# Kernel tuning notes

Hardware: AMD Instinct MI355X
Metric: run time of the kernel (lower is better)

Reference implementation:

```python
import jax, jax.numpy as jnp
import numpy as np

DIM = 768
N_HEADS = 12
HEAD_DIM = DIM // N_HEADS
SCALE = HEAD_DIM ** -0.5


def setup_inputs() -> dict:
    key = jax.random.key(0)
    ks = jax.random.split(key, 5)
    x = jax.random.normal(ks[0], (8, 1024, DIM), dtype=jnp.float32)
    w_qkv = jax.random.normal(ks[1], (DIM, 3 * DIM), dtype=jnp.float32) * (DIM ** -0.5)
    b_qkv = jnp.zeros((3 * DIM,), dtype=jnp.float32)
    w_proj = jax.random.normal(ks[2], (DIM, DIM), dtype=jnp.float32) * (DIM ** -0.5)
    b_proj = jnp.zeros((DIM,), dtype=jnp.float32)
    return {"x": x, "w_qkv": w_qkv, "b_qkv": b_qkv, "w_proj": w_proj, "b_proj": b_proj}


def reference(x, w_qkv, b_qkv, w_proj, b_proj):
    B, N, _ = x.shape
    qkv = x @ w_qkv + b_qkv                       # [B, N, 3*DIM]
    qkv = qkv.reshape(B, N, 3, N_HEADS, HEAD_DIM)
    q = qkv[:, :, 0].transpose(0, 2, 1, 3)        # [B, H, N, D]
    k = qkv[:, :, 1].transpose(0, 2, 1, 3)
    v = qkv[:, :, 2].transpose(0, 2, 1, 3)
    attn = jnp.einsum('bhnd,bhmd->bhnm', q, k) * SCALE
    attn = jax.nn.softmax(attn, axis=-1)
    out = jnp.einsum('bhnm,bhmd->bhnd', attn, v)  # [B, H, N, D]
    out = out.transpose(0, 2, 1, 3).reshape(B, N, DIM)
    return out @ w_proj + b_proj
```

## Files before the change

### kernel.cpp

```cpp
#include <hip/hip_runtime.h>
#include <hip/hip_bf16.h>

#define NHEADS 12
#define HDIM   64
#define SEQ    1024
#define NBATCH 8
#define MODELD 768
#define QKVD   2304
#define BHEADS (NBATCH * NHEADS)

typedef __attribute__((ext_vector_type(8))) short          bf16x8;
typedef __attribute__((ext_vector_type(8))) unsigned short u16x8;
typedef __attribute__((ext_vector_type(4))) unsigned short u16x4;
typedef __attribute__((ext_vector_type(4))) float          f32x4;

static __device__ __forceinline__ unsigned short f2bf(float f) {
  unsigned int u = __float_as_uint(f);
  u += 0x7fffu + ((u >> 16) & 1u);
  return (unsigned short)(u >> 16);
}

static __device__ __forceinline__ unsigned int pk2(float x, float y) {
  __hip_bfloat162 h = __float22bfloat162_rn(make_float2(x, y));
  return *(unsigned int*)&h;
}

static __device__ __forceinline__ void gld_lds16(const void* g, void* l) {
  __builtin_amdgcn_global_load_lds((const __attribute__((address_space(1))) void*)g,
                                   (__attribute__((address_space(3))) void*)l, 16, 0, 0);
}

#define QSC 0.18033688f

static __device__ __forceinline__ void transpose_body(
    const float* __restrict__ in, unsigned short* __restrict__ out,
    int R, int C, int bx, int by, int tid) {
  __shared__ float t[32][33];
  const int c0 = bx * 32, r0 = by * 32;
  const int lr = tid >> 3;
  const int lc = (tid & 7) * 4;
  const float* p = in + (size_t)(r0 + lr) * C + c0 + lc;
  float4 v = *(const float4*)p;
  t[lr][lc]     = v.x;
  t[lr][lc + 1] = v.y;
  t[lr][lc + 2] = v.z;
  t[lr][lc + 3] = v.w;
  __syncthreads();
  unsigned short* q = out + (size_t)(c0 + lr) * R + r0 + lc;
  q[0] = f2bf(t[lc][lr]);
  q[1] = f2bf(t[lc + 1][lr]);
  q[2] = f2bf(t[lc + 2][lr]);
  q[3] = f2bf(t[lc + 3][lr]);
}

__global__ __launch_bounds__(256) void prep(
    const float* __restrict__ x, unsigned short* __restrict__ Xb,
    const float* __restrict__ w_qkv, unsigned short* __restrict__ wqkvT,
    const float* __restrict__ w_proj, unsigned short* __restrict__ wprojT) {
  const int id = blockIdx.x;
  const int tid = threadIdx.x;
  if (id < 3072) {
    const int i = (id * 256 + tid) * 8;
    const float4 a0 = *(const float4*)(x + i);
    const float4 a1 = *(const float4*)(x + i + 4);
    union { unsigned int u[4]; u16x8 v; } w;
    w.u[0] = pk2(a0.x, a0.y); w.u[1] = pk2(a0.z, a0.w);
    w.u[2] = pk2(a1.x, a1.y); w.u[3] = pk2(a1.z, a1.w);
    *(u16x8*)(Xb + i) = w.v;
  } else if (id < 4800) {
    const int u = id - 3072;
    transpose_body(w_qkv, wqkvT, MODELD, QKVD, u % 72, u / 72, tid);
  } else {
    const int u = id - 4800;
    transpose_body(w_proj, wprojT, MODELD, MODELD, u % 24, u / 24, tid);
  }
}

#define GEMM_CORE(AP, BP)                                                      \
  const int tid  = threadIdx.x;                                                \
  const int lane = tid & 63;                                                   \
  const int wave = tid >> 6;                                                   \
  const int wm = wave >> 1, wn = wave & 1;                                     \
  const int fr = lane & 15;                                                    \
  const int fq = lane >> 4;                                                    \
  const int swz = (fr & 7) << 4;                                               \
  const int srow8 = lane >> 3;                                                 \
  const int scb8 = (((lane & 7) ^ srow8) << 4);                                \
  f32x4 acc[4][4] = {};                                                        \
  auto stA = [&](int dbuf, int kb, int R) {                                    \
    gld_lds16(AP + (size_t)(R + srow8) * 1536 + kb + scb8,                     \
              (char*)smem + dbuf * 16384 + R * 128);                           \
  };                                                                           \
  auto stB = [&](int dbuf, int kb, int R) {                                    \
    gld_lds16(BP + (size_t)(R + srow8) * 1536 + kb + scb8,                     \
              (char*)smem + 32768 + dbuf * 16384 + R * 128);                   \
  };                                                                           \
  _Pragma("unroll")                                                            \
  for (int pt = 0; pt < 2; ++pt) {                                             \
    const int kb = pt * 128;                                                   \
    stA(pt, kb, wave * 8);      stA(pt, kb, 32 + wave * 8);                    \
    stA(pt, kb, 64 + wave * 8); stA(pt, kb, 96 + wave * 8);                    \
    stB(pt, kb, wave * 8);      stB(pt, kb, 64 + wave * 8);                    \
    stB(pt, kb, 32 + wave * 8); stB(pt, kb, 96 + wave * 8);                    \
  }                                                                            \
  asm volatile("s_waitcnt vmcnt(8)" ::: "memory");                             \
  __builtin_amdgcn_s_barrier();                                                \
  for (int kt = 0; kt < 12; ++kt) {                                            \
    const int db = kt & 1;                                                     \
    const char* Ad = (const char*)smem + db * 16384;                           \
    const char* Bd = (const char*)smem + 32768 + db * 16384;                   \
    bf16x8 a[4][2], b[4][2];                                                   \
    _Pragma("unroll")                                                          \
    for (int i = 0; i < 4; ++i)                                                \
      _Pragma("unroll")                                                        \
      for (int c = 0; c < 2; ++c)                                              \
        a[i][c] = *(const bf16x8*)(Ad + (wm * 64 + i * 16 + fr) * 128 +        \
                                   ((c * 64 + fq * 16) ^ swz));                \
    _Pragma("unroll")                                                          \
    for (int j = 0; j < 2; ++j)                                                \
      _Pragma("unroll")                                                        \
      for (int c = 0; c < 2; ++c)                                              \
        b[j][c] = *(const bf16x8*)(Bd + (wn * 64 + j * 16 + fr) * 128 +        \
                                   ((c * 64 + fq * 16) ^ swz));                \
    if (kt >= 1 && kt <= 10) {                                                 \
      stB(db ^ 1, (kt + 1) * 128, 32 + wave * 8);                              \
      stB(db ^ 1, (kt + 1) * 128, 96 + wave * 8);                              \
    }                                                                          \
    if (kt < 11) asm volatile("s_waitcnt vmcnt(8)" ::: "memory");              \
    else         asm volatile("s_waitcnt vmcnt(0)" ::: "memory");              \
    __builtin_amdgcn_s_barrier();                                              \
    __builtin_amdgcn_s_setprio(1);                                             \
    _Pragma("unroll")                                                          \
    for (int i = 0; i < 4; ++i)                                                \
      _Pragma("unroll")                                                        \
      for (int j = 0; j < 2; ++j)                                              \
        _Pragma("unroll")                                                      \
        for (int c = 0; c < 2; ++c)                                            \
          acc[i][j] = __builtin_amdgcn_mfma_f32_16x16x32_bf16(                 \
              a[i][c], b[j][c], acc[i][j], 0, 0, 0);                           \
    __builtin_amdgcn_s_setprio(0);                                             \
    __builtin_amdgcn_s_barrier();                                              \
    _Pragma("unroll")                                                          \
    for (int j = 0; j < 2; ++j)                                                \
      _Pragma("unroll")                                                        \
      for (int c = 0; c < 2; ++c)                                              \
        b[2 + j][c] = *(const bf16x8*)(Bd + (wn * 64 + (2 + j) * 16 + fr) *    \
                                       128 + ((c * 64 + fq * 16) ^ swz));      \
    if (kt <= 9) {                                                             \
      const int kb2 = (kt + 2) * 128;                                          \
      stA(db, kb2, wave * 8);      stA(db, kb2, 32 + wave * 8);                \
      stA(db, kb2, 64 + wave * 8); stA(db, kb2, 96 + wave * 8);                \
      stB(db, kb2, wave * 8);      stB(db, kb2, 64 + wave * 8);                \
    }                                                                          \
    if (kt <= 9)       asm volatile("s_waitcnt vmcnt(6)" ::: "memory");        \
    else if (kt == 10) asm volatile("s_waitcnt vmcnt(2)" ::: "memory");        \
    else               asm volatile("s_waitcnt vmcnt(0)" ::: "memory");        \
    __builtin_amdgcn_s_barrier();                                              \
    __builtin_amdgcn_s_setprio(1);                                             \
    _Pragma("unroll")                                                          \
    for (int i = 0; i < 4; ++i)                                                \
      _Pragma("unroll")                                                        \
      for (int j = 0; j < 2; ++j)                                              \
        _Pragma("unroll")                                                      \
        for (int c = 0; c < 2; ++c)                                            \
          acc[i][2 + j] = __builtin_amdgcn_mfma_f32_16x16x32_bf16(             \
              a[i][c], b[2 + j][c], acc[i][2 + j], 0, 0, 0);                   \
    __builtin_amdgcn_s_setprio(0);                                             \
    __builtin_amdgcn_s_barrier();                                              \
  }

__global__ __launch_bounds__(256, 2) void gemm_qkv(
    const unsigned short* __restrict__ Xb, const unsigned short* __restrict__ WT,
    const float* __restrict__ bias,
    unsigned short* __restrict__ Qo, unsigned short* __restrict__ Ko,
    unsigned short* __restrict__ VTo) {
  __shared__ __align__(16) unsigned short smem[32768];
  int flat = blockIdx.x;
  flat = (flat & 7) * 144 + (flat >> 3);
  const int m0 = (flat / 18) * 128;
  const int n0 = (flat % 18) * 128;
  const char* Ap = (const char*)(Xb + (size_t)m0 * MODELD);
  const char* Bp = (const char*)(WT + (size_t)n0 * MODELD);

  GEMM_CORE(Ap, Bp)

  __builtin_amdgcn_s_barrier();
  const int wr = wm * 64, wc = wn * 64;
  const int s = n0 / MODELD;
  if (s < 2) {
    const float qs = (s == 0) ? QSC : 1.0f;
#pragma unroll
    for (int i = 0; i < 4; ++i) {
#pragma unroll
      for (int j = 0; j < 4; ++j) {
        const int col = n0 + wc + j * 16 + fr;
        const int rem = col - s * MODELD;
        const int h = rem >> 6, d = rem & 63;
        const float bv = bias[col];
#pragma unroll
        for (int r = 0; r < 4; ++r) {
          const int row = m0 + wr + i * 16 + fq * 4 + r;
          const int bb = row >> 10, n = row & 1023;
          const int bh = bb * NHEADS + h;
          const unsigned short val = f2bf((acc[i][j][r] + bv) * qs);
          if (s == 0) Qo[((size_t)bh * SEQ + n) * HDIM + d] = val;
          else        Ko[((size_t)bh * SEQ + n) * HDIM + d] = val;
        }
      }
    }
  } else {
    unsigned short* T = smem + wave * 4608;
#pragma unroll
    for (int i = 0; i < 4; ++i) {
#pragma unroll
      for (int j = 0; j < 4; ++j) {
        const int col = n0 + wc + j * 16 + fr;
        const float bv = bias[col];
        const int dl = j * 16 + fr;
        union { unsigned int u[2]; u16x4 v; } pk;
        pk.u[0] = pk2(acc[i][j][0] + bv, acc[i][j][1] + bv);
        pk.u[1] = pk2(acc[i][j][2] + bv, acc[i][j][3] + bv);
        *(u16x4*)&T[dl * 72 + i * 16 + fq * 4] = pk.v;
      }
    }
    asm volatile("s_waitcnt lgkmcnt(0)" ::: "memory");
    const int h  = (n0 + wc - 2 * MODELD) >> 6;
    const int rowb = m0 + wr;
    const int bb = rowb >> 10, nq = rowb & 1023;
    const int bh = bb * NHEADS + h;
    unsigned short* Vb = VTo + ((size_t)bh * HDIM) * SEQ + nq;
#pragma unroll
    for (int u = 0; u < 8; ++u) {
      const int d  = u * 8 + (lane >> 3);
      const int qc = (lane & 7) * 8;
      u16x8 v = *(const u16x8*)&T[d * 72 + qc];
      *(u16x8*)(Vb + (size_t)d * SEQ + qc) = v;
    }
  }
}

__global__ __launch_bounds__(256, 2) void gemm_proj(
    const unsigned short* __restrict__ A, const unsigned short* __restrict__ WT,
    const float* __restrict__ bias, float* __restrict__ Out) {
  __shared__ __align__(16) unsigned short smem[32768];
  int flat = blockIdx.x;
  flat = (flat & 7) * 48 + (flat >> 3);
  const int m0 = (flat / 6) * 128;
  const int n0 = (flat % 6) * 128;
  const char* Ap = (const char*)(A  + (size_t)m0 * MODELD);
  const char* Bp = (const char*)(WT + (size_t)n0 * MODELD);

  GEMM_CORE(Ap, Bp)

  const int wr = wm * 64, wc = wn * 64;
#pragma unroll
  for (int i = 0; i < 4; ++i) {
#pragma unroll
    for (int j = 0; j < 4; ++j) {
      const int col = n0 + wc + j * 16 + fr;
      const float bv = bias[col];
#pragma unroll
      for (int r = 0; r < 4; ++r) {
        const int row = m0 + wr + i * 16 + fq * 4 + r;
        Out[(size_t)row * MODELD + col] = acc[i][j][r] + bv;
      }
    }
  }
}

__global__ __launch_bounds__(256, 3) void attn_fused(
    const unsigned short* __restrict__ Q, const unsigned short* __restrict__ K,
    const unsigned short* __restrict__ VT, unsigned short* __restrict__ AO) {
  __shared__ __align__(16) unsigned short smem[24576];

  const int tid  = threadIdx.x;
  const int lane = tid & 63;
  const int wave = tid >> 6;

  const int flat = blockIdx.y * 8 + blockIdx.x;
  const int xcd = flat & 7, j = flat >> 3;
  const int bh = xcd * 12 + (j >> 3);
  const int qb = j & 7;
  const int b = bh / NHEADS, h = bh % NHEADS;
  const int q0 = qb * 128 + wave * 32;

  const unsigned short* Qp = Q  + (size_t)bh * SEQ * HDIM;
  const unsigned short* Kp = K  + (size_t)bh * SEQ * HDIM;
  const unsigned short* Vp = VT + (size_t)bh * HDIM * SEQ;

  const int fr = lane & 15;
  const int fq = lane >> 4;
  const int swz = (fr & 7) << 4;

  bf16x8 qf[2][2];
#pragma unroll
  for (int g = 0; g < 2; ++g)
#pragma unroll
    for (int c = 0; c < 2; ++c)
      qf[g][c] = *(const bf16x8*)(Qp + (size_t)(q0 + g * 16 + fr) * HDIM + c * 32 + fq * 8);

  const int srow_lo = (lane >> 3);
  const int scx = (((lane & 7) ^ srow_lo) << 4);

  f32x4 acc[2][4] = {};
  f32x4 accl[2] = {};
  bf16x8 ones;
#pragma unroll
  for (int i = 0; i < 8; ++i) ones[i] = (short)0x3F80;

  auto stage = [&](int buf, int kv0) {
    const char* Kb = (const char*)Kp + (size_t)kv0 * 128;
    const char* Vb = (const char*)Vp + (size_t)kv0 * 2;
#pragma unroll
    for (int u = 0; u < 2; ++u) {
      const int i = wave * 2 + u;
      const int r0 = i * 8 + srow_lo;
      gld_lds16(Kb + (size_t)r0 * 128  + scx, (char*)smem + buf * 8192 + i * 1024);
      gld_lds16(Vb + (size_t)r0 * 2048 + scx, (char*)smem + 24576 + buf * 8192 + i * 1024);
    }
  };

  stage(0, 0);
  stage(1, 64);

  int cur = 0;
  for (int t = 0; t < SEQ / 64; ++t) {
    if (t < SEQ / 64 - 1) asm volatile("s_waitcnt vmcnt(4)" ::: "memory");
    else                  asm volatile("s_waitcnt vmcnt(0)" ::: "memory");
    __builtin_amdgcn_s_barrier();
    if (t < SEQ / 64 - 2) {
      int sb = cur + 2; if (sb >= 3) sb -= 3;
      stage(sb, (t + 2) * 64);
    }

    const char* Kt = (const char*)smem + cur * 8192;
    const char* Vt = (const char*)smem + 24576 + cur * 8192;

    bf16x8 kf[4][2];
#pragma unroll
    for (int ng = 0; ng < 4; ++ng)
#pragma unroll
      for (int c = 0; c < 2; ++c)
        kf[ng][c] = *(const bf16x8*)(Kt + (ng * 16 + fr) * 128 + ((c * 64 + fq * 16) ^ swz));

    f32x4 S[2][4] = {};
    __builtin_amdgcn_s_setprio(1);
#pragma unroll
    for (int g = 0; g < 2; ++g)
#pragma unroll
      for (int ng = 0; ng < 4; ++ng)
#pragma unroll
        for (int c = 0; c < 2; ++c)
          S[g][ng] = __builtin_amdgcn_mfma_f32_16x16x32_bf16(kf[ng][c], qf[g][c], S[g][ng], 0, 0, 0);
    __builtin_amdgcn_s_setprio(0);

    bf16x8 pf[2][2];
#pragma unroll
    for (int g = 0; g < 2; ++g) {
      unsigned int u[4][2];
#pragma unroll
      for (int ng = 0; ng < 4; ++ng) {
        const float p0 = __builtin_amdgcn_exp2f(S[g][ng][0]);
        const float p1 = __builtin_amdgcn_exp2f(S[g][ng][1]);
        const float p2 = __builtin_amdgcn_exp2f(S[g][ng][2]);
        const float p3 = __builtin_amdgcn_exp2f(S[g][ng][3]);
        u[ng][0] = pk2(p0, p1);
        u[ng][1] = pk2(p2, p3);
      }
#pragma unroll
      for (int c = 0; c < 2; ++c) {
        union { unsigned int w[4]; bf16x8 v; } pp;
#pragma unroll
        for (int d2 = 0; d2 < 2; ++d2) {
          unsigned int e = u[2 * c][d2], o = u[2 * c + 1][d2];
          asm("v_permlane32_swap_b32 %0, %1" : "+v"(e), "+v"(o));
          asm("v_permlane16_swap_b32 %0, %1" : "+v"(e), "+v"(o));
          pp.w[d2] = e;
          pp.w[2 + d2] = o;
        }
        pf[g][c] = pp.v;
      }
    }

    bf16x8 vf[4][2];
#pragma unroll
    for (int df = 0; df < 4; ++df)
#pragma unroll
      for (int c = 0; c < 2; ++c)
        vf[df][c] = *(const bf16x8*)(Vt + (df * 16 + fr) * 128 + ((c * 64 + fq * 16) ^ swz));

    __builtin_amdgcn_s_setprio(1);
#pragma unroll
    for (int g = 0; g < 2; ++g) {
#pragma unroll
      for (int df = 0; df < 4; ++df)
#pragma unroll
        for (int c = 0; c < 2; ++c)
          acc[g][df] = __builtin_amdgcn_mfma_f32_16x16x32_bf16(pf[g][c], vf[df][c], acc[g][df], 0, 0, 0);
#pragma unroll
      for (int c = 0; c < 2; ++c)
        accl[g] = __builtin_amdgcn_mfma_f32_16x16x32_bf16(pf[g][c], ones, accl[g], 0, 0, 0);
    }
    __builtin_amdgcn_s_setprio(0);

    cur = (cur == 2) ? 0 : cur + 1;
  }

#pragma unroll
  for (int g = 0; g < 2; ++g) {
#pragma unroll
    for (int r = 0; r < 4; ++r) {
      const float inv = 1.0f / accl[g][r];
      const int q = q0 + g * 16 + fq * 4 + r;
      unsigned short* outp = AO + ((size_t)b * SEQ + q) * MODELD + h * HDIM;
#pragma unroll
      for (int df = 0; df < 4; ++df)
        outp[df * 16 + fr] = f2bf(acc[g][df][r] * inv);
    }
  }
}

extern "C" void kernel_launch(void* const* d_in, const int* in_sizes, int n_in,
                              void* d_out, int out_size, void* d_ws, size_t ws_size,
                              hipStream_t stream) {
  const float* x      = (const float*)d_in[0];
  const float* w_qkv  = (const float*)d_in[1];
  const float* b_qkv  = (const float*)d_in[2];
  const float* w_proj = (const float*)d_in[3];
  const float* b_proj = (const float*)d_in[4];
  float* out = (float*)d_out;

  unsigned short* ws = (unsigned short*)d_ws;
  unsigned short* wqkvT  = ws;
  unsigned short* wprojT = wqkvT + (size_t)QKVD * MODELD;
  unsigned short* Qw     = wprojT + (size_t)MODELD * MODELD;
  unsigned short* Kw     = Qw + (size_t)BHEADS * SEQ * HDIM;
  unsigned short* VTw    = Kw + (size_t)BHEADS * SEQ * HDIM;
  unsigned short* AO     = VTw + (size_t)BHEADS * SEQ * HDIM;
  unsigned short* Xb     = AO + (size_t)NBATCH * SEQ * MODELD;

  prep<<<dim3(5376), 256, 0, stream>>>(x, Xb, w_qkv, wqkvT, w_proj, wprojT);
  gemm_qkv<<<dim3((QKVD / 128) * ((NBATCH * SEQ) / 128)), 256, 0, stream>>>(
      Xb, wqkvT, b_qkv, Qw, Kw, VTw);
  attn_fused<<<dim3(SEQ / 128, BHEADS), 256, 0, stream>>>(Qw, Kw, VTw, AO);
  gemm_proj<<<dim3((MODELD / 128) * ((NBATCH * SEQ) / 128)), 256, 0, stream>>>(
      AO, wprojT, b_proj, out);
}
```

Baseline: 94.48 us.

## Make QKV GEMM persistent with atomic ticket tile scheduling

The QKV projection GEMM now launches a fixed 512 persistent workgroups that repeatedly claim 128x128 output tiles from a global atomic counter, instead of one workgroup per tile (1152). The counter is reset in the prep kernel. This aims to reduce the wave-quantization tail (1152 tiles on 256 CUs at 2 blocks per CU) and launch overhead. In exchange it adds an atomic plus two block barriers per tile, and a persistent block cannot overlap one tile's epilogue with the next tile's loads the way independent blocks can.

```diff
diff --git a/kernel.cpp b/kernel.cpp
--- a/kernel.cpp
+++ b/kernel.cpp
@@ -8,6 +8,8 @@
 #define MODELD 768
 #define QKVD   2304
 #define BHEADS (NBATCH * NHEADS)
+#define QKV_TILES 1152
+#define QKV_BLOCKS 512
 
 typedef __attribute__((ext_vector_type(8))) short          bf16x8;
 typedef __attribute__((ext_vector_type(8))) unsigned short u16x8;
@@ -56,9 +58,11 @@
 __global__ __launch_bounds__(256) void prep(
     const float* __restrict__ x, unsigned short* __restrict__ Xb,
     const float* __restrict__ w_qkv, unsigned short* __restrict__ wqkvT,
-    const float* __restrict__ w_proj, unsigned short* __restrict__ wprojT) {
+    const float* __restrict__ w_proj, unsigned short* __restrict__ wprojT,
+    int* __restrict__ ticket) {
   const int id = blockIdx.x;
   const int tid = threadIdx.x;
+  if (id == 0 && tid == 0) *ticket = 0;
   if (id < 3072) {
     const int i = (id * 256 + tid) * 8;
     const float4 a0 = *(const float4*)(x + i);
@@ -76,17 +80,7 @@
   }
 }
 
-#define GEMM_CORE(AP, BP)                                                      \
-  const int tid  = threadIdx.x;                                                \
-  const int lane = tid & 63;                                                   \
-  const int wave = tid >> 6;                                                   \
-  const int wm = wave >> 1, wn = wave & 1;                                     \
-  const int fr = lane & 15;                                                    \
-  const int fq = lane >> 4;                                                    \
-  const int swz = (fr & 7) << 4;                                               \
-  const int srow8 = lane >> 3;                                                 \
-  const int scb8 = (((lane & 7) ^ srow8) << 4);                                \
-  f32x4 acc[4][4] = {};                                                        \
+#define GEMM_CORE_BODY(AP, BP)                                                 \
   auto stA = [&](int dbuf, int kb, int R) {                                    \
     gld_lds16(AP + (size_t)(R + srow8) * 1536 + kb + scb8,                     \
               (char*)smem + dbuf * 16384 + R * 128);                           \
@@ -173,69 +167,89 @@
     const unsigned short* __restrict__ Xb, const unsigned short* __restrict__ WT,
     const float* __restrict__ bias,
     unsigned short* __restrict__ Qo, unsigned short* __restrict__ Ko,
-    unsigned short* __restrict__ VTo) {
+    unsigned short* __restrict__ VTo, int* __restrict__ ticket) {
   __shared__ __align__(16) unsigned short smem[32768];
-  int flat = blockIdx.x;
-  flat = (flat & 7) * 144 + (flat >> 3);
-  const int m0 = (flat / 18) * 128;
-  const int n0 = (flat % 18) * 128;
-  const char* Ap = (const char*)(Xb + (size_t)m0 * MODELD);
-  const char* Bp = (const char*)(WT + (size_t)n0 * MODELD);
-
-  GEMM_CORE(Ap, Bp)
-
-  __builtin_amdgcn_s_barrier();
-  const int wr = wm * 64, wc = wn * 64;
-  const int s = n0 / MODELD;
-  if (s < 2) {
-    const float qs = (s == 0) ? QSC : 1.0f;
-#pragma unroll
-    for (int i = 0; i < 4; ++i) {
-#pragma unroll
-      for (int j = 0; j < 4; ++j) {
-        const int col = n0 + wc + j * 16 + fr;
-        const int rem = col - s * MODELD;
-        const int h = rem >> 6, d = rem & 63;
-        const float bv = bias[col];
-#pragma unroll
-        for (int r = 0; r < 4; ++r) {
-          const int row = m0 + wr + i * 16 + fq * 4 + r;
-          const int bb = row >> 10, n = row & 1023;
-          const int bh = bb * NHEADS + h;
-          const unsigned short val = f2bf((acc[i][j][r] + bv) * qs);
-          if (s == 0) Qo[((size_t)bh * SEQ + n) * HDIM + d] = val;
-          else        Ko[((size_t)bh * SEQ + n) * HDIM + d] = val;
+  __shared__ int tk;
+  const int tid  = threadIdx.x;
+  const int lane = tid & 63;
+  const int wave = tid >> 6;
+  const int wm = wave >> 1, wn = wave & 1;
+  const int fr = lane & 15;
+  const int fq = lane >> 4;
+  const int swz = (fr & 7) << 4;
+  const int srow8 = lane >> 3;
+  const int scb8 = (((lane & 7) ^ srow8) << 4);
+
+  for (;;) {
+    if (tid == 0) tk = atomicAdd(ticket, 1);
+    __syncthreads();
+    const int t = tk;
+    __syncthreads();
+    if (t >= QKV_TILES) break;
+
+    const int flat = (t & 7) * 144 + (t >> 3);
+    const int m0 = (flat / 18) * 128;
+    const int n0 = (flat % 18) * 128;
+    const char* Ap = (const char*)(Xb + (size_t)m0 * MODELD);
+    const char* Bp = (const char*)(WT + (size_t)n0 * MODELD);
+
+    f32x4 acc[4][4] = {};
+    GEMM_CORE_BODY(Ap, Bp)
+
+    __builtin_amdgcn_s_barrier();
+    const int wr = wm * 64, wc = wn * 64;
+    const int s = n0 / MODELD;
+    if (s < 2) {
+      const float qs = (s == 0) ? QSC : 1.0f;
+#pragma unroll
+      for (int i = 0; i < 4; ++i) {
+#pragma unroll
+        for (int j = 0; j < 4; ++j) {
+          const int col = n0 + wc + j * 16 + fr;
+          const int rem = col - s * MODELD;
+          const int h = rem >> 6, d = rem & 63;
+          const float bv = bias[col];
+#pragma unroll
+          for (int r = 0; r < 4; ++r) {
+            const int row = m0 + wr + i * 16 + fq * 4 + r;
+            const int bb = row >> 10, n = row & 1023;
+            const int bh = bb * NHEADS + h;
+            const unsigned short val = f2bf((acc[i][j][r] + bv) * qs);
+            if (s == 0) Qo[((size_t)bh * SEQ + n) * HDIM + d] = val;
+            else        Ko[((size_t)bh * SEQ + n) * HDIM + d] = val;
+          }
         }
       }
-    }
-  } else {
-    unsigned short* T = smem + wave * 4608;
-#pragma unroll
-    for (int i = 0; i < 4; ++i) {
-#pragma unroll
-      for (int j = 0; j < 4; ++j) {
-        const int col = n0 + wc + j * 16 + fr;
-        const float bv = bias[col];
-        const int dl = j * 16 + fr;
-        union { unsigned int u[2]; u16x4 v; } pk;
-        pk.u[0] = pk2(acc[i][j][0] + bv, acc[i][j][1] + bv);
-        pk.u[1] = pk2(acc[i][j][2] + bv, acc[i][j][3] + bv);
-        *(u16x4*)&T[dl * 72 + i * 16 + fq * 4] = pk.v;
-      }
-    }
-    asm volatile("s_waitcnt lgkmcnt(0)" ::: "memory");
-    const int h  = (n0 + wc - 2 * MODELD) >> 6;
-    const int rowb = m0 + wr;
-    const int bb = rowb >> 10, nq = rowb & 1023;
-    const int bh = bb * NHEADS + h;
-    unsigned short* Vb = VTo + ((size_t)bh * HDIM) * SEQ + nq;
-#pragma unroll
-    for (int u = 0; u < 8; ++u) {
-      const int d  = u * 8 + (lane >> 3);
-      const int qc = (lane & 7) * 8;
-      u16x8 v = *(const u16x8*)&T[d * 72 + qc];
-      *(u16x8*)(Vb + (size_t)d * SEQ + qc) = v;
-    }
+    } else {
+      unsigned short* T = smem + wave * 4608;
+#pragma unroll
+      for (int i = 0; i < 4; ++i) {
+#pragma unroll
+        for (int j = 0; j < 4; ++j) {
+          const int col = n0 + wc + j * 16 + fr;
+          const float bv = bias[col];
+          const int dl = j * 16 + fr;
+          union { unsigned int u[2]; u16x4 v; } pk;
+          pk.u[0] = pk2(acc[i][j][0] + bv, acc[i][j][1] + bv);
+          pk.u[1] = pk2(acc[i][j][2] + bv, acc[i][j][3] + bv);
+          *(u16x4*)&T[dl * 72 + i * 16 + fq * 4] = pk.v;
+        }
+      }
+      asm volatile("s_waitcnt lgkmcnt(0)" ::: "memory");
+      const int h  = (n0 + wc - 2 * MODELD) >> 6;
+      const int rowb = m0 + wr;
+      const int bb = rowb >> 10, nq = rowb & 1023;
+      const int bh = bb * NHEADS + h;
+      unsigned short* Vb = VTo + ((size_t)bh * HDIM) * SEQ + nq;
+#pragma unroll
+      for (int u = 0; u < 8; ++u) {
+        const int d  = u * 8 + (lane >> 3);
+        const int qc = (lane & 7) * 8;
+        u16x8 v = *(const u16x8*)&T[d * 72 + qc];
+        *(u16x8*)(Vb + (size_t)d * SEQ + qc) = v;
+      }
+    }
+    __syncthreads();
   }
 }
 
@@ -243,6 +257,15 @@
     const unsigned short* __restrict__ A, const unsigned short* __restrict__ WT,
     const float* __restrict__ bias, float* __restrict__ Out) {
   __shared__ __align__(16) unsigned short smem[32768];
+  const int tid  = threadIdx.x;
+  const int lane = tid & 63;
+  const int wave = tid >> 6;
+  const int wm = wave >> 1, wn = wave & 1;
+  const int fr = lane & 15;
+  const int fq = lane >> 4;
+  const int swz = (fr & 7) << 4;
+  const int srow8 = lane >> 3;
+  const int scb8 = (((lane & 7) ^ srow8) << 4);
   int flat = blockIdx.x;
   flat = (flat & 7) * 48 + (flat >> 3);
   const int m0 = (flat / 6) * 128;
@@ -250,7 +273,8 @@
   const char* Ap = (const char*)(A  + (size_t)m0 * MODELD);
   const char* Bp = (const char*)(WT + (size_t)n0 * MODELD);
 
-  GEMM_CORE(Ap, Bp)
+  f32x4 acc[4][4] = {};
+  GEMM_CORE_BODY(Ap, Bp)
 
   const int wr = wm * 64, wc = wn * 64;
 #pragma unroll
@@ -438,10 +462,11 @@
   unsigned short* VTw    = Kw + (size_t)BHEADS * SEQ * HDIM;
   unsigned short* AO     = VTw + (size_t)BHEADS * SEQ * HDIM;
   unsigned short* Xb     = AO + (size_t)NBATCH * SEQ * MODELD;
-
-  prep<<<dim3(5376), 256, 0, stream>>>(x, Xb, w_qkv, wqkvT, w_proj, wprojT);
-  gemm_qkv<<<dim3((QKVD / 128) * ((NBATCH * SEQ) / 128)), 256, 0, stream>>>(
-      Xb, wqkvT, b_qkv, Qw, Kw, VTw);
+  int* ticket = (int*)(Xb + (size_t)NBATCH * SEQ * MODELD);
+
+  prep<<<dim3(5376), 256, 0, stream>>>(x, Xb, w_qkv, wqkvT, w_proj, wprojT, ticket);
+  gemm_qkv<<<dim3(QKV_BLOCKS), 256, 0, stream>>>(
+      Xb, wqkvT, b_qkv, Qw, Kw, VTw, ticket);
   attn_fused<<<dim3(SEQ / 128, BHEADS), 256, 0, stream>>>(Qw, Kw, VTw, AO);
   gemm_proj<<<dim3((MODELD / 128) * ((NBATCH * SEQ) / 128)), 256, 0, stream>>>(
       AO, wprojT, b_proj, out);
```

Result: slower. 110.3 us (+16.7%).

## Shrink GEMM N-tile from 128 to 96 for better wave balance

Applied to the files above, without the earlier changes.

Both the QKV and output-projection GEMMs switch from 128x128 to 128x96 block tiles. B loading, LDS sizing, wait counts, the MFMA inner loops and the epilogues (including the V-transpose path, which now handles tiles straddling heads) are all adapted. The aim is more blocks so the grid fills the CUs in whole waves and leaves less tail idle time. In exchange, each block reuses A less per FLOP and its epilogue indexing is slightly more complex.

```diff
diff --git a/kernel.cpp b/kernel.cpp
--- a/kernel.cpp
+++ b/kernel.cpp
@@ -76,7 +76,7 @@
   }
 }
 
-#define GEMM_CORE(AP, BP)                                                      \
+#define GEMM_CORE96(AP, BP)                                                    \
   const int tid  = threadIdx.x;                                                \
   const int lane = tid & 63;                                                   \
   const int wave = tid >> 6;                                                   \
@@ -86,30 +86,34 @@
   const int swz = (fr & 7) << 4;                                               \
   const int srow8 = lane >> 3;                                                 \
   const int scb8 = (((lane & 7) ^ srow8) << 4);                                \
-  f32x4 acc[4][4] = {};                                                        \
+  const int ReB0 = wave * 8;                         \
+  const int ReB1 = 48 + wave * 8;                    \
+  const int RlB  = ((wave & 2) ? 64 : 32) + wave * 8;      \
+  f32x4 acc[4][3] = {};                                                        \
   auto stA = [&](int dbuf, int kb, int R) {                                    \
     gld_lds16(AP + (size_t)(R + srow8) * 1536 + kb + scb8,                     \
               (char*)smem + dbuf * 16384 + R * 128);                           \
   };                                                                           \
   auto stB = [&](int dbuf, int kb, int R) {                                    \
     gld_lds16(BP + (size_t)(R + srow8) * 1536 + kb + scb8,                     \
-              (char*)smem + 32768 + dbuf * 16384 + R * 128);                   \
+              (char*)smem + 32768 + dbuf * 12288 + R * 128);                   \
   };                                                                           \
   _Pragma("unroll")                                                            \
   for (int pt = 0; pt < 2; ++pt) {                                             \
     const int kb = pt * 128;                                                   \
     stA(pt, kb, wave * 8);      stA(pt, kb, 32 + wave * 8);                    \
     stA(pt, kb, 64 + wave * 8); stA(pt, kb, 96 + wave * 8);                    \
-    stB(pt, kb, wave * 8);      stB(pt, kb, 64 + wave * 8);                    \
-    stB(pt, kb, 32 + wave * 8); stB(pt, kb, 96 + wave * 8);                    \
+    stB(pt, kb, ReB0);          stB(pt, kb, ReB1);                             \
+    stB(pt, kb, RlB);                                                          \
   }                                                                            \
-  asm volatile("s_waitcnt vmcnt(8)" ::: "memory");                             \
+  asm volatile("s_waitcnt vmcnt(7)" ::: "memory");                             \
   __builtin_amdgcn_s_barrier();                                                \
   for (int kt = 0; kt < 12; ++kt) {                                            \
     const int db = kt & 1;                                                     \
     const char* Ad = (const char*)smem + db * 16384;                           \
-    const char* Bd = (const char*)smem + 32768 + db * 16384;                   \
-    bf16x8 a[4][2], b[4][2];                                                   \
+    const char* Bd = (const char*)smem + 32768 + db * 12288;                   \
+    bf16x8 a[4][2], b[3][2];                                                   \
+                                                        \
     _Pragma("unroll")                                                          \
     for (int i = 0; i < 4; ++i)                                                \
       _Pragma("unroll")                                                        \
@@ -120,13 +124,10 @@
     for (int j = 0; j < 2; ++j)                                                \
       _Pragma("unroll")                                                        \
       for (int c = 0; c < 2; ++c)                                              \
-        b[j][c] = *(const bf16x8*)(Bd + (wn * 64 + j * 16 + fr) * 128 +        \
+        b[j][c] = *(const bf16x8*)(Bd + (wn * 48 + j * 16 + fr) * 128 +        \
                                    ((c * 64 + fq * 16) ^ swz));                \
-    if (kt >= 1 && kt <= 10) {                                                 \
-      stB(db ^ 1, (kt + 1) * 128, 32 + wave * 8);                              \
-      stB(db ^ 1, (kt + 1) * 128, 96 + wave * 8);                              \
-    }                                                                          \
-    if (kt < 11) asm volatile("s_waitcnt vmcnt(8)" ::: "memory");              \
+    if (kt >= 1 && kt <= 10) stB(db ^ 1, (kt + 1) * 128, RlB);                 \
+    if (kt < 11) asm volatile("s_waitcnt vmcnt(7)" ::: "memory");              \
     else         asm volatile("s_waitcnt vmcnt(0)" ::: "memory");              \
     __builtin_amdgcn_s_barrier();                                              \
     __builtin_amdgcn_s_setprio(1);                                             \
@@ -140,31 +141,28 @@
               a[i][c], b[j][c], acc[i][j], 0, 0, 0);                           \
     __builtin_amdgcn_s_setprio(0);                                             \
     __builtin_amdgcn_s_barrier();                                              \
+                                                        \
     _Pragma("unroll")                                                          \
-    for (int j = 0; j < 2; ++j)                                                \
-      _Pragma("unroll")                                                        \
-      for (int c = 0; c < 2; ++c)                                              \
-        b[2 + j][c] = *(const bf16x8*)(Bd + (wn * 64 + (2 + j) * 16 + fr) *    \
-                                       128 + ((c * 64 + fq * 16) ^ swz));      \
+    for (int c = 0; c < 2; ++c)                                                \
+      b[2][c] = *(const bf16x8*)(Bd + (wn * 48 + 32 + fr) * 128 +              \
+                                 ((c * 64 + fq * 16) ^ swz));                  \
     if (kt <= 9) {                                                             \
       const int kb2 = (kt + 2) * 128;                                          \
       stA(db, kb2, wave * 8);      stA(db, kb2, 32 + wave * 8);                \
       stA(db, kb2, 64 + wave * 8); stA(db, kb2, 96 + wave * 8);                \
-      stB(db, kb2, wave * 8);      stB(db, kb2, 64 + wave * 8);                \
+      stB(db, kb2, ReB0);          stB(db, kb2, ReB1);                         \
     }                                                                          \
     if (kt <= 9)       asm volatile("s_waitcnt vmcnt(6)" ::: "memory");        \
-    else if (kt == 10) asm volatile("s_waitcnt vmcnt(2)" ::: "memory");        \
+    else if (kt == 10) asm volatile("s_waitcnt vmcnt(1)" ::: "memory");        \
     else               asm volatile("s_waitcnt vmcnt(0)" ::: "memory");        \
     __builtin_amdgcn_s_barrier();                                              \
     __builtin_amdgcn_s_setprio(1);                                             \
     _Pragma("unroll")                                                          \
     for (int i = 0; i < 4; ++i)                                                \
       _Pragma("unroll")                                                        \
-      for (int j = 0; j < 2; ++j)                                              \
-        _Pragma("unroll")                                                      \
-        for (int c = 0; c < 2; ++c)                                            \
-          acc[i][2 + j] = __builtin_amdgcn_mfma_f32_16x16x32_bf16(             \
-              a[i][c], b[2 + j][c], acc[i][2 + j], 0, 0, 0);                   \
+      for (int c = 0; c < 2; ++c)                                              \
+        acc[i][2] = __builtin_amdgcn_mfma_f32_16x16x32_bf16(                   \
+            a[i][c], b[2][c], acc[i][2], 0, 0, 0);                             \
     __builtin_amdgcn_s_setprio(0);                                             \
     __builtin_amdgcn_s_barrier();                                              \
   }
@@ -174,32 +172,31 @@
     const float* __restrict__ bias,
     unsigned short* __restrict__ Qo, unsigned short* __restrict__ Ko,
     unsigned short* __restrict__ VTo) {
-  __shared__ __align__(16) unsigned short smem[32768];
+  __shared__ __align__(16) unsigned short smem[28672];
   int flat = blockIdx.x;
-  flat = (flat & 7) * 144 + (flat >> 3);
-  const int m0 = (flat / 18) * 128;
-  const int n0 = (flat % 18) * 128;
+  flat = (flat & 7) * 192 + (flat >> 3);
+  const int m0 = (flat / 24) * 128;
+  const int n0 = (flat % 24) * 96;
   const char* Ap = (const char*)(Xb + (size_t)m0 * MODELD);
   const char* Bp = (const char*)(WT + (size_t)n0 * MODELD);
 
-  GEMM_CORE(Ap, Bp)
+  GEMM_CORE96(Ap, Bp)
 
   __builtin_amdgcn_s_barrier();
-  const int wr = wm * 64, wc = wn * 64;
   const int s = n0 / MODELD;
   if (s < 2) {
     const float qs = (s == 0) ? QSC : 1.0f;
 #pragma unroll
     for (int i = 0; i < 4; ++i) {
 #pragma unroll
-      for (int j = 0; j < 4; ++j) {
-        const int col = n0 + wc + j * 16 + fr;
+      for (int j = 0; j < 3; ++j) {
+        const int col = n0 + wn * 48 + j * 16 + fr;
         const int rem = col - s * MODELD;
         const int h = rem >> 6, d = rem & 63;
         const float bv = bias[col];
 #pragma unroll
         for (int r = 0; r < 4; ++r) {
-          const int row = m0 + wr + i * 16 + fq * 4 + r;
+          const int row = m0 + wm * 64 + i * 16 + fq * 4 + r;
           const int bb = row >> 10, n = row & 1023;
           const int bh = bb * NHEADS + h;
           const unsigned short val = f2bf((acc[i][j][r] + bv) * qs);
@@ -209,12 +206,12 @@
       }
     }
   } else {
-    unsigned short* T = smem + wave * 4608;
+    unsigned short* T = smem + wave * 3456;
 #pragma unroll
     for (int i = 0; i < 4; ++i) {
 #pragma unroll
-      for (int j = 0; j < 4; ++j) {
-        const int col = n0 + wc + j * 16 + fr;
+      for (int j = 0; j < 3; ++j) {
+        const int col = n0 + wn * 48 + j * 16 + fr;
         const float bv = bias[col];
         const int dl = j * 16 + fr;
         union { unsigned int u[2]; u16x4 v; } pk;
@@ -224,17 +221,17 @@
       }
     }
     asm volatile("s_waitcnt lgkmcnt(0)" ::: "memory");
-    const int h  = (n0 + wc - 2 * MODELD) >> 6;
-    const int rowb = m0 + wr;
+    const int rowb = m0 + wm * 64;
     const int bb = rowb >> 10, nq = rowb & 1023;
-    const int bh = bb * NHEADS + h;
-    unsigned short* Vb = VTo + ((size_t)bh * HDIM) * SEQ + nq;
-#pragma unroll
-    for (int u = 0; u < 8; ++u) {
-      const int d  = u * 8 + (lane >> 3);
+#pragma unroll
+    for (int u = 0; u < 6; ++u) {
+      const int dslot = u * 8 + (lane >> 3);
       const int qc = (lane & 7) * 8;
-      u16x8 v = *(const u16x8*)&T[d * 72 + qc];
-      *(u16x8*)(Vb + (size_t)d * SEQ + qc) = v;
+      const int rem = n0 + wn * 48 + dslot - 2 * MODELD;
+      const int h = rem >> 6, d = rem & 63;
+      const int bh = bb * NHEADS + h;
+      u16x8 v = *(const u16x8*)&T[dslot * 72 + qc];
+      *(u16x8*)(VTo + ((size_t)bh * HDIM + d) * SEQ + nq + qc) = v;
     }
   }
 }
@@ -242,26 +239,25 @@
 __global__ __launch_bounds__(256, 2) void gemm_proj(
     const unsigned short* __restrict__ A, const unsigned short* __restrict__ WT,
     const float* __restrict__ bias, float* __restrict__ Out) {
-  __shared__ __align__(16) unsigned short smem[32768];
+  __shared__ __align__(16) unsigned short smem[28672];
   int flat = blockIdx.x;
-  flat = (flat & 7) * 48 + (flat >> 3);
-  const int m0 = (flat / 6) * 128;
-  const int n0 = (flat % 6) * 128;
+  flat = (flat & 7) * 64 + (flat >> 3);
+  const int m0 = (flat / 8) * 128;
+  const int n0 = (flat % 8) * 96;
   const char* Ap = (const char*)(A  + (size_t)m0 * MODELD);
   const char* Bp = (const char*)(WT + (size_t)n0 * MODELD);
 
-  GEMM_CORE(Ap, Bp)
-
-  const int wr = wm * 64, wc = wn * 64;
+  GEMM_CORE96(Ap, Bp)
+
 #pragma unroll
   for (int i = 0; i < 4; ++i) {
 #pragma unroll
-    for (int j = 0; j < 4; ++j) {
-      const int col = n0 + wc + j * 16 + fr;
+    for (int j = 0; j < 3; ++j) {
+      const int col = n0 + wn * 48 + j * 16 + fr;
       const float bv = bias[col];
 #pragma unroll
       for (int r = 0; r < 4; ++r) {
-        const int row = m0 + wr + i * 16 + fq * 4 + r;
+        const int row = m0 + wm * 64 + i * 16 + fq * 4 + r;
         Out[(size_t)row * MODELD + col] = acc[i][j][r] + bv;
       }
     }
@@ -440,9 +436,9 @@
   unsigned short* Xb     = AO + (size_t)NBATCH * SEQ * MODELD;
 
   prep<<<dim3(5376), 256, 0, stream>>>(x, Xb, w_qkv, wqkvT, w_proj, wprojT);
-  gemm_qkv<<<dim3((QKVD / 128) * ((NBATCH * SEQ) / 128)), 256, 0, stream>>>(
+  gemm_qkv<<<dim3((QKVD / 96) * ((NBATCH * SEQ) / 128)), 256, 0, stream>>>(
       Xb, wqkvT, b_qkv, Qw, Kw, VTw);
   attn_fused<<<dim3(SEQ / 128, BHEADS), 256, 0, stream>>>(Qw, Kw, VTw, AO);
-  gemm_proj<<<dim3((MODELD / 128) * ((NBATCH * SEQ) / 128)), 256, 0, stream>>>(
+  gemm_proj<<<dim3((MODELD / 96) * ((NBATCH * SEQ) / 128)), 256, 0, stream>>>(
       AO, wprojT, b_proj, out);
 }
```

New measurement: 93.68 us (median of 2 runs). Within noise of the previous version (-0.8%).
